# Kernel tuning notes

Measured on AMD Instinct MI355X. Metric: run time of the kernel, lower is better.

The kernel has to match this reference:

```python
import jax, jax.numpy as jnp
import numpy as np
from jax import lax

BN_EPS = 1e-5

def dwconv(x, w, dilation):
    # x: [N,C,H,W], w: [C,1,k,k] depthwise; SAME padding = (r*(k-1)+1)//2
    k = w.shape[-1]
    pad = (dilation * (k - 1) + 1) // 2
    return lax.conv_general_dilated(
        x, w, window_strides=(1, 1), padding=[(pad, pad), (pad, pad)],
        rhs_dilation=(dilation, dilation), feature_group_count=x.shape[1],
        dimension_numbers=('NCHW', 'OIHW', 'NCHW'))

def bn_eval(y, gamma, beta, mean, var):
    # inference BatchNorm2d over channel dim; params: [C]
    inv = gamma * lax.rsqrt(var + BN_EPS)
    return y * inv[None, :, None, None] + (beta - mean * inv)[None, :, None, None]

def setup_inputs() -> dict:
    key = jax.random.key(0)
    ks = jax.random.split(key, 13)
    C = 384
    x = jax.random.normal(ks[0], (16, C, 56, 56), jnp.float32)
    w_lk = jax.random.normal(ks[1], (C, 1, 13, 13), jnp.float32) * 0.05
    w_b0 = jax.random.normal(ks[2], (C, 1, 5, 5), jnp.float32) * 0.05
    w_b1 = jax.random.normal(ks[3], (C, 1, 7, 7), jnp.float32) * 0.05
    w_b2 = jax.random.normal(ks[4], (C, 1, 7, 7), jnp.float32) * 0.05
    w_b3 = jax.random.normal(ks[5], (C, 1, 3, 3), jnp.float32) * 0.05
    w_b4 = jax.random.normal(ks[6], (C, 1, 3, 3), jnp.float32) * 0.05
    w_b5 = jax.random.normal(ks[7], (C, 1, 3, 3), jnp.float32) * 0.05
    bn_gamma = jax.random.uniform(ks[8], (7, C), jnp.float32, 0.5, 1.5)
    bn_beta = jax.random.normal(ks[9], (7, C), jnp.float32) * 0.1
    bn_mean = jax.random.normal(ks[10], (7, C), jnp.float32) * 0.1
    bn_var = jax.random.uniform(ks[11], (7, C), jnp.float32, 0.5, 1.5)
    return dict(x=x, w_lk=w_lk, w_b0=w_b0, w_b1=w_b1, w_b2=w_b2, w_b3=w_b3,
                w_b4=w_b4, w_b5=w_b5, bn_gamma=bn_gamma, bn_beta=bn_beta,
                bn_mean=bn_mean, bn_var=bn_var)

def reference(x, w_lk, w_b0, w_b1, w_b2, w_b3, w_b4, w_b5,
              bn_gamma, bn_beta, bn_mean, bn_var):
    # DilatedReparamBlock (kernel_size=13, non-deploy):
    # out = BN(dw13(x)) + sum_i BN_i(dw_{k_i, r_i}(x))
    dilates = (1, 1, 2, 3, 4, 5)
    branch_ws = (w_b0, w_b1, w_b2, w_b3, w_b4, w_b5)
    out = bn_eval(dwconv(x, w_lk, 1), bn_gamma[0], bn_beta[0], bn_mean[0], bn_var[0])
    for i, (w, r) in enumerate(zip(branch_ws, dilates)):
        j = i + 1
        out = out + bn_eval(dwconv(x, w, r), bn_gamma[j], bn_beta[j], bn_mean[j], bn_var[j])
    return out
```

## Files before the change

### kernel.cpp

```cpp
#include <hip/hip_runtime.h>
#include <hip/hip_fp16.h>


#define CCH 384
#define SP 56
#define PWH 72
#define NPLANES (16*384)

__device__ __forceinline__ float rfl(float v) {
    return __int_as_float(__builtin_amdgcn_readfirstlane(__float_as_int(v)));
}

typedef __attribute__((ext_vector_type(4))) unsigned int u32x4;

__global__ __launch_bounds__(64, 2) void drb_conv13_r12(
    const float* __restrict__ x,
    const float* __restrict__ w_lk, const float* __restrict__ w_b0,
    const float* __restrict__ w_b1, const float* __restrict__ w_b2,
    const float* __restrict__ w_b3, const float* __restrict__ w_b4,
    const float* __restrict__ w_b5,
    const float* __restrict__ gamma, const float* __restrict__ beta,
    const float* __restrict__ mean, const float* __restrict__ var,
    float* __restrict__ out)
{
    __shared__ __align__(16) __half sxh[68 * PWH];
    __shared__ __align__(16) float sw[13 * 16];

    const int plane = blockIdx.x;
    const int c = plane % CCH;
    const int tid = threadIdx.x;
    const float* __restrict__ xp = x + (size_t)plane * (SP * SP);

    float4 stage[13];
    #pragma unroll
    for (int k = 0; k < 13; k++) {
        int i4 = tid + 64 * k;
        if (i4 < SP * SP / 4) stage[k] = ((const float4*)xp)[i4];
    }

    float S[7];
    float bias = 0.f;
    #pragma unroll
    for (int j = 0; j < 7; j++) {
        float inv = gamma[j * CCH + c] * rsqrtf(var[j * CCH + c] + 1e-5f);
        S[j] = inv;
        bias += beta[j * CCH + c] - mean[j * CCH + c] * inv;
    }

    {
        u32x4 z = {0u, 0u, 0u, 0u};
        #pragma unroll
        for (int k = 0; k < 10; k++) {
            int i = tid + 64 * k;
            if (i < (68 * PWH) / 8) ((u32x4*)sxh)[i] = z;
        }
    }

    #pragma unroll
    for (int k = 0; k < 4; k++) {
        int t = tid + 64 * k;
        if (t < 13 * 16) {
            int ky = t >> 4, kx = t & 15;
            float w = 0.f;
            if (kx < 13) {
                w = S[0] * w_lk[c * 169 + ky * 13 + kx];
                if (ky >= 4 && ky <= 8 && kx >= 4 && kx <= 8)
                    w += S[1] * w_b0[c * 25 + (ky - 4) * 5 + (kx - 4)];
                if (ky >= 3 && ky <= 9 && kx >= 3 && kx <= 9)
                    w += S[2] * w_b1[c * 49 + (ky - 3) * 7 + (kx - 3)];
                if (!(ky & 1) && !(kx & 1))
                    w += S[3] * w_b2[c * 49 + (ky >> 1) * 7 + (kx >> 1)];
                if (ky >= 3 && ky <= 9 && (ky - 3) % 3 == 0 &&
                    kx >= 3 && kx <= 9 && (kx - 3) % 3 == 0)
                    w += S[4] * w_b3[c * 9 + ((ky - 3) / 3) * 3 + (kx - 3) / 3];
                if (ky >= 2 && ky <= 10 && (ky - 2) % 4 == 0 &&
                    kx >= 2 && kx <= 10 && (kx - 2) % 4 == 0)
                    w += S[5] * w_b4[c * 9 + ((ky - 2) / 4) * 3 + (kx - 2) / 4];
                if (ky >= 1 && ky <= 11 && (ky - 1) % 5 == 0 &&
                    kx >= 1 && kx <= 11 && (kx - 1) % 5 == 0)
                    w += S[6] * w_b5[c * 9 + ((ky - 1) / 5) * 3 + (kx - 1) / 5];
            }
            sw[t] = w;
        }
    }

    #pragma unroll
    for (int k = 0; k < 13; k++) {
        int i4 = tid + 64 * k;
        if (i4 < SP * SP / 4) {
            float4 v = stage[k];
            int r = i4 / 14;
            int col = (i4 - r * 14) * 4;
            __half2* d2 = (__half2*)&sxh[(r + 6) * PWH + col + 8];
            d2[0] = __floats2half2_rn(v.x, v.y);
            d2[1] = __floats2half2_rn(v.z, v.w);
        }
    }
    __syncthreads();

    const int xg = tid & 7;
    const int yg = tid >> 3;
    const int xgc = (xg < 7) ? xg : 3;
    const int Yb = yg * 7;
    const __half* __restrict__ sbaseh = &sxh[Yb * PWH + 8 * xgc];

    float acc[7][8];
    #pragma unroll
    for (int r = 0; r < 7; r++)
        #pragma unroll
        for (int j = 0; j < 8; j++) acc[r][j] = 0.f;

#define LOADROW(WF, ROWP)                                                   \
    {                                                                       \
        const u32x4* cp_ = (const u32x4*)(ROWP);                            \
        u32x4 c0_ = cp_[0];                                                 \
        const __half2* p0_ = (const __half2*)&c0_;                          \
        float2 f_;                                                          \
        f_ = __half22float2(p0_[1]); WF[0] = f_.x; WF[1] = f_.y;            \
        f_ = __half22float2(p0_[2]); WF[2] = f_.x; WF[3] = f_.y;            \
        f_ = __half22float2(p0_[3]); WF[4] = f_.x; WF[5] = f_.y;            \
        u32x4 c1_ = cp_[1];                                                 \
        const __half2* p1_ = (const __half2*)&c1_;                          \
        f_ = __half22float2(p1_[0]); WF[6] = f_.x; WF[7] = f_.y;            \
        f_ = __half22float2(p1_[1]); WF[8] = f_.x; WF[9] = f_.y;            \
        f_ = __half22float2(p1_[2]); WF[10] = f_.x; WF[11] = f_.y;          \
        f_ = __half22float2(p1_[3]); WF[12] = f_.x; WF[13] = f_.y;          \
        u32x4 c2_ = cp_[2];                                                 \
        const __half2* p2_ = (const __half2*)&c2_;                          \
        f_ = __half22float2(p2_[0]); WF[14] = f_.x; WF[15] = f_.y;          \
        f_ = __half22float2(p2_[1]); WF[16] = f_.x; WF[17] = f_.y;          \
        f_ = __half22float2(p2_[2]); WF[18] = f_.x; WF[19] = f_.y;          \
    }

    #pragma unroll 1
    for (int k0 = 0; k0 < 12; k0 += 4) {
        float w[4][13];
        #pragma unroll
        for (int dy = 0; dy < 4; dy++) {
            const float* wr = &sw[(k0 + dy) * 16];
            #pragma unroll
            for (int q = 0; q < 3; q++) {
                float4 t = ((const float4*)wr)[q];
                w[dy][4*q+0] = rfl(t.x); w[dy][4*q+1] = rfl(t.y);
                w[dy][4*q+2] = rfl(t.z); w[dy][4*q+3] = rfl(t.w);
            }
            w[dy][12] = rfl(wr[12]);
        }
        #pragma unroll
        for (int i = 0; i < 10; i++) {
            float win[20];
            LOADROW(win, sbaseh + (k0 + i) * PWH);
            #pragma unroll
            for (int dy = 0; dy < 4; dy++) {
                const int r = i - dy;
                if (r >= 0 && r < 7) {
                    #pragma unroll
                    for (int kx = 0; kx < 13; kx++) {
                        const float wv = w[dy][kx];
                        #pragma unroll
                        for (int j = 0; j < 8; j++)
                            acc[r][j] = fmaf(wv, win[kx + j], acc[r][j]);
                    }
                }
            }
        }
    }
    {
        float w12[13];
        const float* wr = &sw[12 * 16];
        #pragma unroll
        for (int q = 0; q < 3; q++) {
            float4 t = ((const float4*)wr)[q];
            w12[4*q+0] = rfl(t.x); w12[4*q+1] = rfl(t.y);
            w12[4*q+2] = rfl(t.z); w12[4*q+3] = rfl(t.w);
        }
        w12[12] = rfl(wr[12]);
        #pragma unroll
        for (int i = 0; i < 7; i++) {
            float win[20];
            LOADROW(win, sbaseh + (12 + i) * PWH);
            #pragma unroll
            for (int kx = 0; kx < 13; kx++) {
                const float wv = w12[kx];
                #pragma unroll
                for (int j = 0; j < 8; j++)
                    acc[i][j] = fmaf(wv, win[kx + j], acc[i][j]);
            }
        }
    }
#undef LOADROW

    if (xg < 7) {
        float* op = out + (size_t)plane * (SP * SP) + Yb * SP + 8 * xg;
        #pragma unroll
        for (int r = 0; r < 7; r++) {
            float4 v0 = make_float4(acc[r][0] + bias, acc[r][1] + bias,
                                    acc[r][2] + bias, acc[r][3] + bias);
            float4 v1 = make_float4(acc[r][4] + bias, acc[r][5] + bias,
                                    acc[r][6] + bias, acc[r][7] + bias);
            *(float4*)(op + r * SP) = v0;
            *(float4*)(op + r * SP + 4) = v1;
        }
    }
}

extern "C" void kernel_launch(void* const* d_in, const int* in_sizes, int n_in,
                              void* d_out, int out_size, void* d_ws, size_t ws_size,
                              hipStream_t stream) {
    const float* x    = (const float*)d_in[0];
    const float* w_lk = (const float*)d_in[1];
    const float* w_b0 = (const float*)d_in[2];
    const float* w_b1 = (const float*)d_in[3];
    const float* w_b2 = (const float*)d_in[4];
    const float* w_b3 = (const float*)d_in[5];
    const float* w_b4 = (const float*)d_in[6];
    const float* w_b5 = (const float*)d_in[7];
    const float* bn_g = (const float*)d_in[8];
    const float* bn_b = (const float*)d_in[9];
    const float* bn_m = (const float*)d_in[10];
    const float* bn_v = (const float*)d_in[11];
    float* out = (float*)d_out;

    drb_conv13_r12<<<dim3(NPLANES), dim3(64), 0, stream>>>(
        x, w_lk, w_b0, w_b1, w_b2, w_b3, w_b4, w_b5,
        bn_g, bn_b, bn_m, bn_v, out);
}
```

Measured before the change: 244.5 us.

## Use packed fp16 dot2 instructions for the depthwise conv inner loop

Merged weights are converted to packed half2 pairs in shared memory. The inner loop now does v_dot2 (fp16x2 dot with fp32 accumulate) on shifted packed input words, where before it unpacked every input row to fp32 and issued scalar FMAs. This halves the multiply-add instruction count and removes the half-to-float conversions. The cost is a few shift/or ops per row to build odd-aligned pairs, plus lower precision because the weights are now rounded to fp16.

```diff
diff --git a/kernel.cpp b/kernel.cpp
--- a/kernel.cpp
+++ b/kernel.cpp
@@ -7,13 +7,28 @@
 #define PWH 72
 #define NPLANES (16*384)
 
+typedef __attribute__((ext_vector_type(4))) unsigned int u32x4;
+typedef _Float16 hf2 __attribute__((ext_vector_type(2)));
+
 __device__ __forceinline__ float rfl(float v) {
     return __int_as_float(__builtin_amdgcn_readfirstlane(__float_as_int(v)));
 }
-
-typedef __attribute__((ext_vector_type(4))) unsigned int u32x4;
-
-__global__ __launch_bounds__(64, 2) void drb_conv13_r12(
+__device__ __forceinline__ unsigned rflu(unsigned v) {
+    return (unsigned)__builtin_amdgcn_readfirstlane((int)v);
+}
+__device__ __forceinline__ hf2 as_hf2(unsigned v) {
+    union { unsigned u; hf2 h; } x; x.u = v; return x.h;
+}
+__device__ __forceinline__ float dot2h(float c, unsigned x, unsigned w) {
+#if __has_builtin(__builtin_amdgcn_fdot2)
+    return __builtin_amdgcn_fdot2(as_hf2(x), as_hf2(w), c, false);
+#else
+    hf2 xh = as_hf2(x), wh = as_hf2(w);
+    return fmaf((float)xh.x, (float)wh.x, fmaf((float)xh.y, (float)wh.y, c));
+#endif
+}
+
+__global__ __launch_bounds__(64, 2) void drb_conv13_r14(
     const float* __restrict__ x,
     const float* __restrict__ w_lk, const float* __restrict__ w_b0,
     const float* __restrict__ w_b1, const float* __restrict__ w_b2,
@@ -25,6 +40,7 @@
 {
     __shared__ __align__(16) __half sxh[68 * PWH];
     __shared__ __align__(16) float sw[13 * 16];
+    __shared__ __align__(16) unsigned swh[13 * 8];
 
     const int plane = blockIdx.x;
     const int c = plane % CCH;
@@ -85,6 +101,19 @@
     }
 
     #pragma unroll
+    for (int k = 0; k < 2; k++) {
+        int t = tid + 64 * k;
+        if (t < 13 * 8) {
+            int ky = t >> 3, p = t & 7;
+            float w0 = sw[ky * 16 + 2 * p];
+            float w1 = sw[ky * 16 + 2 * p + 1];
+            hf2 hh; hh.x = (_Float16)w0; hh.y = (_Float16)w1;
+            union { hf2 h; unsigned u; } cv; cv.h = hh;
+            swh[t] = cv.u;
+        }
+    }
+
+    #pragma unroll
     for (int k = 0; k < 13; k++) {
         int i4 = tid + 64 * k;
         if (i4 < SP * SP / 4) {
@@ -110,85 +139,73 @@
         #pragma unroll
         for (int j = 0; j < 8; j++) acc[r][j] = 0.f;
 
-#define LOADROW(WF, ROWP)                                                   \
+#define ROWDOT(ROWP, DYN, WPA)                                              \
     {                                                                       \
         const u32x4* cp_ = (const u32x4*)(ROWP);                            \
-        u32x4 c0_ = cp_[0];                                                 \
-        const __half2* p0_ = (const __half2*)&c0_;                          \
-        float2 f_;                                                          \
-        f_ = __half22float2(p0_[1]); WF[0] = f_.x; WF[1] = f_.y;            \
-        f_ = __half22float2(p0_[2]); WF[2] = f_.x; WF[3] = f_.y;            \
-        f_ = __half22float2(p0_[3]); WF[4] = f_.x; WF[5] = f_.y;            \
-        u32x4 c1_ = cp_[1];                                                 \
-        const __half2* p1_ = (const __half2*)&c1_;                          \
-        f_ = __half22float2(p1_[0]); WF[6] = f_.x; WF[7] = f_.y;            \
-        f_ = __half22float2(p1_[1]); WF[8] = f_.x; WF[9] = f_.y;            \
-        f_ = __half22float2(p1_[2]); WF[10] = f_.x; WF[11] = f_.y;          \
-        f_ = __half22float2(p1_[3]); WF[12] = f_.x; WF[13] = f_.y;          \
-        u32x4 c2_ = cp_[2];                                                 \
-        const __half2* p2_ = (const __half2*)&c2_;                          \
-        f_ = __half22float2(p2_[0]); WF[14] = f_.x; WF[15] = f_.y;          \
-        f_ = __half22float2(p2_[1]); WF[16] = f_.x; WF[17] = f_.y;          \
-        f_ = __half22float2(p2_[2]); WF[18] = f_.x; WF[19] = f_.y;          \
+        u32x4 c0_ = cp_[0], c1_ = cp_[1], c2_ = cp_[2];                     \
+        unsigned e_[12], o_[11];                                            \
+        e_[0]=c0_.x; e_[1]=c0_.y; e_[2]=c0_.z; e_[3]=c0_.w;                 \
+        e_[4]=c1_.x; e_[5]=c1_.y; e_[6]=c1_.z; e_[7]=c1_.w;                 \
+        e_[8]=c2_.x; e_[9]=c2_.y; e_[10]=c2_.z; e_[11]=c2_.w;               \
+        _Pragma("unroll")                                                   \
+        for (int t_ = 1; t_ <= 10; t_++)                                    \
+            o_[t_] = (e_[t_] >> 16) | (e_[t_ + 1] << 16);                   \
+        _Pragma("unroll")                                                   \
+        for (int dy_ = 0; dy_ < (DYN); dy_++) {                             \
+            const int r_ = i - dy_ - RBASE;                                 \
+            if (r_ >= 0 && r_ < 7) {                                        \
+                _Pragma("unroll")                                           \
+                for (int j_ = 0; j_ < 8; j_++) {                            \
+                    float a_ = acc[r_][j_];                                 \
+                    _Pragma("unroll")                                       \
+                    for (int p_ = 0; p_ < 7; p_++) {                        \
+                        unsigned xa_ = (j_ & 1) ? o_[((j_ + 1) >> 1) + p_]  \
+                                                : e_[(j_ >> 1) + 1 + p_];   \
+                        a_ = dot2h(a_, xa_, WPA[dy_][p_]);                  \
+                    }                                                       \
+                    acc[r_][j_] = a_;                                       \
+                }                                                           \
+            }                                                               \
+        }                                                                   \
     }
 
     #pragma unroll 1
     for (int k0 = 0; k0 < 12; k0 += 4) {
-        float w[4][13];
+        unsigned wp[4][7];
         #pragma unroll
         for (int dy = 0; dy < 4; dy++) {
-            const float* wr = &sw[(k0 + dy) * 16];
-            #pragma unroll
-            for (int q = 0; q < 3; q++) {
-                float4 t = ((const float4*)wr)[q];
-                w[dy][4*q+0] = rfl(t.x); w[dy][4*q+1] = rfl(t.y);
-                w[dy][4*q+2] = rfl(t.z); w[dy][4*q+3] = rfl(t.w);
-            }
-            w[dy][12] = rfl(wr[12]);
-        }
+            const u32x4* wr4 = (const u32x4*)&swh[(k0 + dy) * 8];
+            u32x4 A = wr4[0], B = wr4[1];
+            wp[dy][0] = rflu(A.x); wp[dy][1] = rflu(A.y);
+            wp[dy][2] = rflu(A.z); wp[dy][3] = rflu(A.w);
+            wp[dy][4] = rflu(B.x); wp[dy][5] = rflu(B.y);
+            wp[dy][6] = rflu(B.z);
+        }
+        #define RBASE 0
         #pragma unroll
         for (int i = 0; i < 10; i++) {
-            float win[20];
-            LOADROW(win, sbaseh + (k0 + i) * PWH);
-            #pragma unroll
-            for (int dy = 0; dy < 4; dy++) {
-                const int r = i - dy;
-                if (r >= 0 && r < 7) {
-                    #pragma unroll
-                    for (int kx = 0; kx < 13; kx++) {
-                        const float wv = w[dy][kx];
-                        #pragma unroll
-                        for (int j = 0; j < 8; j++)
-                            acc[r][j] = fmaf(wv, win[kx + j], acc[r][j]);
-                    }
-                }
-            }
-        }
+            const __half* rp = sbaseh + (k0 + i) * PWH;
+            ROWDOT(rp, 4, wp)
+        }
+        #undef RBASE
     }
     {
-        float w12[13];
-        const float* wr = &sw[12 * 16];
-        #pragma unroll
-        for (int q = 0; q < 3; q++) {
-            float4 t = ((const float4*)wr)[q];
-            w12[4*q+0] = rfl(t.x); w12[4*q+1] = rfl(t.y);
-            w12[4*q+2] = rfl(t.z); w12[4*q+3] = rfl(t.w);
-        }
-        w12[12] = rfl(wr[12]);
+        unsigned wpT[1][7];
+        const u32x4* wr4 = (const u32x4*)&swh[12 * 8];
+        u32x4 A = wr4[0], B = wr4[1];
+        wpT[0][0] = rflu(A.x); wpT[0][1] = rflu(A.y);
+        wpT[0][2] = rflu(A.z); wpT[0][3] = rflu(A.w);
+        wpT[0][4] = rflu(B.x); wpT[0][5] = rflu(B.y);
+        wpT[0][6] = rflu(B.z);
+        #define RBASE 0
         #pragma unroll
         for (int i = 0; i < 7; i++) {
-            float win[20];
-            LOADROW(win, sbaseh + (12 + i) * PWH);
-            #pragma unroll
-            for (int kx = 0; kx < 13; kx++) {
-                const float wv = w12[kx];
-                #pragma unroll
-                for (int j = 0; j < 8; j++)
-                    acc[i][j] = fmaf(wv, win[kx + j], acc[i][j]);
-            }
-        }
-    }
-#undef LOADROW
+            const __half* rp = sbaseh + (12 + i) * PWH;
+            ROWDOT(rp, 1, wpT)
+        }
+        #undef RBASE
+    }
+#undef ROWDOT
 
     if (xg < 7) {
         float* op = out + (size_t)plane * (SP * SP) + Yb * SP + 8 * xg;
@@ -221,7 +238,7 @@
     const float* bn_v = (const float*)d_in[11];
     float* out = (float*)d_out;
 
-    drb_conv13_r12<<<dim3(NPLANES), dim3(64), 0, stream>>>(
+    drb_conv13_r14<<<dim3(NPLANES), dim3(64), 0, stream>>>(
         x, w_lk, w_b0, w_b1, w_b2, w_b3, w_b4, w_b5,
         bn_g, bn_b, bn_m, bn_v, out);
 }
```

After: 231.1 us. 1.06x faster.
